# Performance work log

Measured on AMD Instinct MI355X. Metric: run time of the kernel, lower is better.

## Reference

```python
import jax, jax.numpy as jnp
import numpy as np

N = 100000       # num nodes
E = 1000000      # num edges
D_IN = 128       # input feature dim
D_H = 64         # hidden = output dim
EPS = 1e-5       # GraphNorm eps
SLOPE = 0.2      # LeakyReLU negative slope


def _glorot(key, shape):
    lim = float(np.sqrt(6.0 / (shape[0] + shape[1])))
    return jax.random.uniform(key, shape, jnp.float32, -lim, lim)


def setup_inputs() -> dict:
    key = jax.random.key(0)
    ks = jax.random.split(key, 6)
    return {
        "x": jax.random.normal(ks[0], (N, D_IN), jnp.float32),
        "edge_index": jax.random.randint(ks[1], (2, E), 0, N),
        "W_in": _glorot(ks[2], (D_IN, D_H)),
        "b_in": jnp.zeros((D_H,), jnp.float32),
        "W1": _glorot(ks[3], (D_H, D_H)),
        "b1": jnp.zeros((D_H,), jnp.float32),
        "gn1_alpha": jnp.ones((D_H,), jnp.float32),
        "gn1_gamma": jnp.ones((D_H,), jnp.float32),
        "gn1_beta": jnp.zeros((D_H,), jnp.float32),
        "W2": _glorot(ks[4], (D_H, D_H)),
        "b2": jnp.zeros((D_H,), jnp.float32),
        "gn2_alpha": jnp.ones((D_H,), jnp.float32),
        "gn2_gamma": jnp.ones((D_H,), jnp.float32),
        "gn2_beta": jnp.zeros((D_H,), jnp.float32),
    }


def gcn_conv(x, W, b, src, dst):
    # GCNConv with added self-loops and symmetric normalization:
    # out = D^{-1/2} (A + I) D^{-1/2} (x W) + b
    xw = x @ W                                                 # [N, D]
    ones = jnp.ones((src.shape[0],), x.dtype)
    deg = jax.ops.segment_sum(ones, dst, num_segments=x.shape[0]) + 1.0  # +1 self-loop
    dinv = jax.lax.rsqrt(deg)                                  # [N]
    coef = dinv[src] * dinv[dst]                               # [E]
    agg = jax.ops.segment_sum(xw[src] * coef[:, None], dst, num_segments=x.shape[0])
    return agg + xw * (dinv * dinv)[:, None] + b


def graph_norm(x, alpha, gamma, beta):
    # PyG GraphNorm over a single graph: per-feature mean/var over all nodes
    mean = jnp.mean(x, axis=0)
    c = x - alpha * mean
    var = jnp.mean(c * c, axis=0)
    return gamma * c * jax.lax.rsqrt(var + EPS) + beta


def reference(x, edge_index, W_in, b_in, W1, b1, gn1_alpha, gn1_gamma, gn1_beta,
              W2, b2, gn2_alpha, gn2_gamma, gn2_beta):
    src, dst = edge_index[0], edge_index[1]
    h = x @ W_in + b_in                                        # input projection
    h = graph_norm(gcn_conv(h, W1, b1, src, dst), gn1_alpha, gn1_gamma, gn1_beta)
    h = jnp.where(h > 0, h, SLOPE * h)                         # LeakyReLU(0.2); dropout=eval (identity)
    h = graph_norm(gcn_conv(h, W2, b2, src, dst), gn2_alpha, gn2_gamma, gn2_beta)
    return h                                                    # [N, D_H]
```

## Files before the change

### kernel.cpp

```cpp
#include <hip/hip_runtime.h>
#include <stdint.h>

#define N_NODES 100000
#define N_EDGES 1000000
#define D_IN 128
#define D_H 64
#define EPS 1e-5f
#define SLOPE 0.2f

typedef unsigned short u16;
typedef unsigned int u32;

__device__ __forceinline__ float bf2f(u16 u) {
    union { u32 i; float f; } v; v.i = ((u32)u) << 16; return v.f;
}
__device__ __forceinline__ u16 f2bf(float f) {
    union { float f; u32 i; } v; v.f = f;
    u32 r = (v.i + 0x7fffu + ((v.i >> 16) & 1u)) >> 16;
    return (u16)r;
}
__device__ __forceinline__ bool is_f32(const void* flagp) {
    return *(const u32*)flagp == 0x3F800000u;
}
__device__ __forceinline__ float loadf(const void* p, size_t i, bool m) {
    return m ? ((const float*)p)[i] : bf2f(((const u16*)p)[i]);
}

__global__ void kprep(const void* __restrict__ W_in, const void* __restrict__ b_in,
                      const void* __restrict__ W1, const void* __restrict__ flagp,
                      float* __restrict__ Wc, float* __restrict__ bc)
{
    bool m = is_f32(flagp);
    int c = blockIdx.x;
    int t = threadIdx.x;
    __shared__ float w1c[D_H];
    if (t < D_H) w1c[t] = loadf(W1, t * D_H + c, m);
    __syncthreads();
    float acc = 0.f;
    #pragma unroll 8
    for (int j = 0; j < D_H; j++) acc += loadf(W_in, t * D_H + j, m) * w1c[j];
    Wc[t * D_H + c] = acc;
    if (t == 0) {
        float b = 0.f;
        for (int j = 0; j < D_H; j++) b += loadf(b_in, j, m) * w1c[j];
        bc[c] = b;
    }
}

__global__ void kfill(const int* __restrict__ ei, int* __restrict__ cnt,
                      int* __restrict__ bucket)
{
    int e = blockIdx.x * blockDim.x + threadIdx.x;
    if (e >= N_EDGES) return;
    int s = ei[e];
    int d = ei[N_EDGES + e];
    int slot = atomicAdd(&cnt[d], 1);
    if (slot < 64) bucket[(size_t)d * 64 + slot] = s;
}

__global__ void kdinv(const int* __restrict__ cnt, float* __restrict__ dinv,
                      u16* __restrict__ xwb_pad)
{
    int i = blockIdx.x * blockDim.x + threadIdx.x;
    if (i < D_H) xwb_pad[(size_t)N_NODES * D_H + i] = 0;
    if (i >= N_NODES) return;
    dinv[i] = rsqrtf((float)cnt[i] + 1.0f);
}

__global__ __launch_bounds__(256) void kgemm1(const void* __restrict__ x,
        const float* __restrict__ Wc, const float* __restrict__ bc,
        const float* __restrict__ dinv, const void* __restrict__ flagp,
        u16* __restrict__ xwb)
{
    bool m = is_f32(flagp);
    __shared__ __align__(16) u16 xs[64 * 132];
    __shared__ float WL[D_IN * D_H];
    int tid = threadIdx.x;
    int row0 = blockIdx.x * 64;
    for (int i = tid; i < D_IN * D_H / 4; i += 256)
        ((float4*)WL)[i] = ((const float4*)Wc)[i];
    for (int i = tid; i < 64 * 32; i += 256) {
        int r = i >> 5, kq = (i & 31) * 4;
        int gr = row0 + r;
        ushort4 u = make_ushort4(0, 0, 0, 0);
        if (gr < N_NODES) {
            if (m) {
                float4 v = *(const float4*)((const float*)x + (size_t)gr * D_IN + kq);
                u = make_ushort4(f2bf(v.x), f2bf(v.y), f2bf(v.z), f2bf(v.w));
            } else {
                u = *(const ushort4*)((const u16*)x + (size_t)gr * D_IN + kq);
            }
        }
        *(ushort4*)(xs + r * 132 + kq) = u;
    }
    __syncthreads();
    int tx = tid & 15, ry = tid >> 4;
    float4 bcv = ((const float4*)bc)[tx];
    float acc[4][4];
    #pragma unroll
    for (int j = 0; j < 4; j++) { acc[j][0] = bcv.x; acc[j][1] = bcv.y; acc[j][2] = bcv.z; acc[j][3] = bcv.w; }
    #pragma unroll 4
    for (int k = 0; k < D_IN; k += 2) {
        float4 w0 = *(const float4*)(WL + k * D_H + tx * 4);
        float4 w1 = *(const float4*)(WL + (k + 1) * D_H + tx * 4);
        #pragma unroll
        for (int j = 0; j < 4; j++) {
            u32 p = *(const u32*)(xs + (ry * 4 + j) * 132 + k);
            float xl = bf2f((u16)(p & 0xffffu));
            float xh = bf2f((u16)(p >> 16));
            acc[j][0] += xl * w0.x; acc[j][1] += xl * w0.y; acc[j][2] += xl * w0.z; acc[j][3] += xl * w0.w;
            acc[j][0] += xh * w1.x; acc[j][1] += xh * w1.y; acc[j][2] += xh * w1.z; acc[j][3] += xh * w1.w;
        }
    }
    #pragma unroll
    for (int j = 0; j < 4; j++) {
        int gr = row0 + ry * 4 + j;
        if (gr < N_NODES) {
            float ds = dinv[gr];
            *(ushort4*)(xwb + (size_t)gr * D_H + tx * 4) =
                make_ushort4(f2bf(acc[j][0] * ds), f2bf(acc[j][1] * ds),
                             f2bf(acc[j][2] * ds), f2bf(acc[j][3] * ds));
        }
    }
}

__global__ __launch_bounds__(256) void kagg(const u16* __restrict__ xwb,
        const float* __restrict__ dinv, const int* __restrict__ cnt,
        const int* __restrict__ bucket, const void* __restrict__ bvec,
        const void* __restrict__ flagp, u16* __restrict__ ybuf,
        float* __restrict__ accum)
{
    bool m = is_f32(flagp);
    __shared__ int s_src[4][8][68];
    __shared__ __align__(16) float red[8][64];
    int tid = threadIdx.x;
    int wv = tid >> 6, L = tid & 63;
    int r = L >> 4, c = L & 15;
    int node0 = blockIdx.x * 32 + wv * 8;

    int cnt8 = cnt[node0 + (L & 7)];
    float di8 = dinv[node0 + (L & 7)];
    int deg[8]; float dd[8];
    #pragma unroll
    for (int t = 0; t < 8; t++) {
        deg[t] = min(__builtin_amdgcn_readlane(cnt8, t), 64);
        dd[t] = __uint_as_float(__builtin_amdgcn_readlane(__float_as_uint(di8), t));
    }
    #pragma unroll
    for (int t = 0; t < 8; t++) {
        int i = node0 + t;
        int sl = N_NODES;
        if (L < deg[t]) sl = bucket[(size_t)i * 64 + L];
        else if (L == deg[t]) sl = i;
        s_src[wv][t][L] = sl;
        if (L < 4) s_src[wv][t][64 + L] = (deg[t] == 64 && L == 0) ? i : N_NODES;
    }
    float b4[4];
    #pragma unroll
    for (int j = 0; j < 4; j++) b4[j] = loadf(bvec, c * 4 + j, m);

    float ls0 = 0, ls1 = 0, ls2 = 0, ls3 = 0;
    float lq0 = 0, lq1 = 0, lq2 = 0, lq3 = 0;

    #pragma unroll
    for (int tp = 0; tp < 8; tp += 2) {
        int na = deg[tp] + 1, nb = deg[tp + 1] + 1;
        int smax = max(na, nb);
        float a0 = 0, a1 = 0, a2 = 0, a3 = 0;
        float e0 = 0, e1 = 0, e2 = 0, e3 = 0;
        const int* sa = s_src[wv][tp];
        const int* sb = s_src[wv][tp + 1];
        for (int s = 0; s < smax; s += 4) {
            int ia = sa[s + r];
            int ib = sb[s + r];
            uint2 da = *(const uint2*)(xwb + (size_t)ia * D_H + c * 4);
            uint2 db = *(const uint2*)(xwb + (size_t)ib * D_H + c * 4);
            a0 += __uint_as_float(da.x << 16);
            a1 += __uint_as_float(da.x & 0xffff0000u);
            a2 += __uint_as_float(da.y << 16);
            a3 += __uint_as_float(da.y & 0xffff0000u);
            e0 += __uint_as_float(db.x << 16);
            e1 += __uint_as_float(db.x & 0xffff0000u);
            e2 += __uint_as_float(db.y << 16);
            e3 += __uint_as_float(db.y & 0xffff0000u);
        }
        a0 += __shfl_xor(a0, 16); a1 += __shfl_xor(a1, 16);
        a2 += __shfl_xor(a2, 16); a3 += __shfl_xor(a3, 16);
        e0 += __shfl_xor(e0, 16); e1 += __shfl_xor(e1, 16);
        e2 += __shfl_xor(e2, 16); e3 += __shfl_xor(e3, 16);
        a0 += __shfl_xor(a0, 32); a1 += __shfl_xor(a1, 32);
        a2 += __shfl_xor(a2, 32); a3 += __shfl_xor(a3, 32);
        e0 += __shfl_xor(e0, 32); e1 += __shfl_xor(e1, 32);
        e2 += __shfl_xor(e2, 32); e3 += __shfl_xor(e3, 32);
        float ya0 = dd[tp] * a0 + b4[0];
        float ya1 = dd[tp] * a1 + b4[1];
        float ya2 = dd[tp] * a2 + b4[2];
        float ya3 = dd[tp] * a3 + b4[3];
        float ye0 = dd[tp + 1] * e0 + b4[0];
        float ye1 = dd[tp + 1] * e1 + b4[1];
        float ye2 = dd[tp + 1] * e2 + b4[2];
        float ye3 = dd[tp + 1] * e3 + b4[3];
        if (r == 0) {
            *(ushort4*)(ybuf + (size_t)(node0 + tp) * D_H + c * 4) =
                make_ushort4(f2bf(ya0), f2bf(ya1), f2bf(ya2), f2bf(ya3));
            *(ushort4*)(ybuf + (size_t)(node0 + tp + 1) * D_H + c * 4) =
                make_ushort4(f2bf(ye0), f2bf(ye1), f2bf(ye2), f2bf(ye3));
            ls0 += ya0 + ye0; ls1 += ya1 + ye1;
            ls2 += ya2 + ye2; ls3 += ya3 + ye3;
            lq0 += ya0 * ya0 + ye0 * ye0; lq1 += ya1 * ya1 + ye1 * ye1;
            lq2 += ya2 * ya2 + ye2 * ye2; lq3 += ya3 * ya3 + ye3 * ye3;
        }
    }
    if (r == 0) {
        *(float4*)&red[wv * 2][c * 4] = make_float4(ls0, ls1, ls2, ls3);
        *(float4*)&red[wv * 2 + 1][c * 4] = make_float4(lq0, lq1, lq2, lq3);
    }
    __syncthreads();
    if (tid < 64) {
        atomicAdd(&accum[tid],      red[0][tid] + red[2][tid] + red[4][tid] + red[6][tid]);
        atomicAdd(&accum[64 + tid], red[1][tid] + red[3][tid] + red[5][tid] + red[7][tid]);
    }
}

__global__ void kparams(const float* __restrict__ accum, const void* __restrict__ alpha,
        const void* __restrict__ gamma, const void* __restrict__ beta,
        const void* __restrict__ flagp, float* __restrict__ params)
{
    bool m = is_f32(flagp);
    int f = threadIdx.x;
    float mean = accum[f] * (1.0f / N_NODES);
    float al = loadf(alpha, f, m);
    float var = accum[64 + f] * (1.0f / N_NODES) - mean * mean * al * (2.0f - al);
    var = fmaxf(var, 0.f);
    float a = loadf(gamma, f, m) * rsqrtf(var + EPS);
    params[f] = a;
    params[64 + f] = loadf(beta, f, m) - a * al * mean;
}

__global__ __launch_bounds__(256) void kgemm2(const u16* __restrict__ y1b,
        const void* __restrict__ W2, const float* __restrict__ params,
        const float* __restrict__ dinv, const void* __restrict__ flagp,
        u16* __restrict__ xwb)
{
    bool m = is_f32(flagp);
    __shared__ __align__(16) u16 hs[64 * 68];
    __shared__ float WL[D_H * D_H];
    __shared__ float aL[64], cL[64];
    int tid = threadIdx.x;
    if (tid < 64) { aL[tid] = params[tid]; cL[tid] = params[64 + tid]; }
    for (int i = tid; i < D_H * D_H; i += 256) WL[i] = loadf(W2, i, m);
    __syncthreads();
    int row0 = blockIdx.x * 64;
    for (int i = tid; i < 64 * 16; i += 256) {
        int r = i >> 4, kq = (i & 15) * 4;
        int gr = row0 + r;
        ushort4 u = make_ushort4(0, 0, 0, 0);
        if (gr < N_NODES) u = *(const ushort4*)(y1b + (size_t)gr * D_H + kq);
        float h0 = aL[kq + 0] * bf2f(u.x) + cL[kq + 0]; h0 = h0 > 0.f ? h0 : SLOPE * h0;
        float h1 = aL[kq + 1] * bf2f(u.y) + cL[kq + 1]; h1 = h1 > 0.f ? h1 : SLOPE * h1;
        float h2 = aL[kq + 2] * bf2f(u.z) + cL[kq + 2]; h2 = h2 > 0.f ? h2 : SLOPE * h2;
        float h3 = aL[kq + 3] * bf2f(u.w) + cL[kq + 3]; h3 = h3 > 0.f ? h3 : SLOPE * h3;
        *(ushort4*)(hs + r * 68 + kq) = make_ushort4(f2bf(h0), f2bf(h1), f2bf(h2), f2bf(h3));
    }
    __syncthreads();
    int tx = tid & 15, ry = tid >> 4;
    float acc[4][4] = {};
    #pragma unroll 4
    for (int k = 0; k < D_H; k += 2) {
        float4 w0 = *(const float4*)(WL + k * D_H + tx * 4);
        float4 w1 = *(const float4*)(WL + (k + 1) * D_H + tx * 4);
        #pragma unroll
        for (int j = 0; j < 4; j++) {
            u32 p = *(const u32*)(hs + (ry * 4 + j) * 68 + k);
            float xl = bf2f((u16)(p & 0xffffu));
            float xh = bf2f((u16)(p >> 16));
            acc[j][0] += xl * w0.x; acc[j][1] += xl * w0.y; acc[j][2] += xl * w0.z; acc[j][3] += xl * w0.w;
            acc[j][0] += xh * w1.x; acc[j][1] += xh * w1.y; acc[j][2] += xh * w1.z; acc[j][3] += xh * w1.w;
        }
    }
    #pragma unroll
    for (int j = 0; j < 4; j++) {
        int gr = row0 + ry * 4 + j;
        if (gr < N_NODES) {
            float ds = dinv[gr];
            *(ushort4*)(xwb + (size_t)gr * D_H + tx * 4) =
                make_ushort4(f2bf(acc[j][0] * ds), f2bf(acc[j][1] * ds),
                             f2bf(acc[j][2] * ds), f2bf(acc[j][3] * ds));
        }
    }
}

__global__ void kout(const u16* __restrict__ y2b, const float* __restrict__ params2,
                     const void* __restrict__ flagp, void* __restrict__ out)
{
    bool m = is_f32(flagp);
    int idx = blockIdx.x * blockDim.x + threadIdx.x;
    if (idx >= N_NODES * D_H) return;
    int f = idx & 63;
    float v = params2[f] * bf2f(y2b[idx]) + params2[64 + f];
    if (m) ((float*)out)[idx] = v;
    else   ((u16*)out)[idx] = f2bf(v);
}

extern "C" void kernel_launch(void* const* d_in, const int* in_sizes, int n_in,
                              void* d_out, int out_size, void* d_ws, size_t ws_size,
                              hipStream_t stream)
{
    const void* x    = d_in[0];
    const int*  ei   = (const int*)d_in[1];
    const void* W_in = d_in[2];
    const void* b_in = d_in[3];
    const void* W1   = d_in[4];
    const void* b1   = d_in[5];
    const void* gn1a = d_in[6];
    const void* gn1g = d_in[7];
    const void* gn1b = d_in[8];
    const void* W2   = d_in[9];
    const void* b2   = d_in[10];
    const void* gn2a = d_in[11];
    const void* gn2g = d_in[12];
    const void* gn2b = d_in[13];

    char* ws = (char*)d_ws;
    int*   cnt    = (int*)(ws + 0);
    float* accum  = (float*)(ws + 400000);
    float* params = (float*)(ws + 401024);
    float* bc     = (float*)(ws + 402048);
    float* Wc     = (float*)(ws + 402432);
    float* dinv   = (float*)(ws + 435200);
    int*   bucket = (int*)(ws + 1235200);
    u16*   bufA   = (u16*)(ws + 26835200);
    u16*   bufB   = (u16*)(ws + 39635456);

    hipMemsetAsync(ws, 0, 400000 + 1024, stream);

    kprep<<<64, 128, 0, stream>>>(W_in, b_in, W1, gn1a, Wc, bc);
    kfill<<<(N_EDGES + 255) / 256, 256, 0, stream>>>(ei, cnt, bucket);
    kdinv<<<(N_NODES + 255) / 256, 256, 0, stream>>>(cnt, dinv, bufA);
    kgemm1<<<(N_NODES + 63) / 64, 256, 0, stream>>>(x, Wc, bc, dinv, gn1a, bufA);
    kagg<<<N_NODES / 32, 256, 0, stream>>>(bufA, dinv, cnt, bucket, b1, gn1a, bufB, accum);
    kparams<<<1, 64, 0, stream>>>(accum, gn1a, gn1g, gn1b, gn1a, params);
    kgemm2<<<(N_NODES + 63) / 64, 256, 0, stream>>>(bufB, W2, params, dinv, gn1a, bufA);
    kagg<<<N_NODES / 32, 256, 0, stream>>>(bufA, dinv, cnt, bucket, b2, gn1a, bufB, accum + 128);
    kparams<<<1, 64, 0, stream>>>(accum + 128, gn2a, gn2g, gn2b, gn1a, params + 128);
    kout<<<(N_NODES * D_H + 255) / 256, 256, 0, stream>>>(bufB, params + 128, gn1a, d_out);
}
```

Before: 449.9 us.

## Prefetch first 16 neighbor rows per node into registers before aggregation

Measured after the change: 439.5 us. 2.3% less time.

```diff
diff --git a/kernel.cpp b/kernel.cpp
--- a/kernel.cpp
+++ b/kernel.cpp
@@ -131,7 +131,6 @@
         float* __restrict__ accum)
 {
     bool m = is_f32(flagp);
-    __shared__ int s_src[4][8][68];
     __shared__ __align__(16) float red[8][64];
     int tid = threadIdx.x;
     int wv = tid >> 6, L = tid & 63;
@@ -146,15 +145,31 @@
         deg[t] = min(__builtin_amdgcn_readlane(cnt8, t), 64);
         dd[t] = __uint_as_float(__builtin_amdgcn_readlane(__float_as_uint(di8), t));
     }
-    #pragma unroll
-    for (int t = 0; t < 8; t++) {
-        int i = node0 + t;
-        int sl = N_NODES;
-        if (L < deg[t]) sl = bucket[(size_t)i * 64 + L];
-        else if (L == deg[t]) sl = i;
-        s_src[wv][t][L] = sl;
-        if (L < 4) s_src[wv][t][64 + L] = (deg[t] == 64 && L == 0) ? i : N_NODES;
-    }
+
+    int bsl[8][4];
+    #pragma unroll
+    for (int t = 0; t < 8; t++) {
+        const int* bk = bucket + (size_t)(node0 + t) * 64;
+        #pragma unroll
+        for (int q = 0; q < 4; q++) bsl[t][q] = bk[q * 4 + r];
+    }
+    #pragma unroll
+    for (int t = 0; t < 8; t++) {
+        #pragma unroll
+        for (int q = 0; q < 4; q++) {
+            int si = q * 4 + r;
+            bsl[t][q] = (si < deg[t]) ? bsl[t][q]
+                      : ((si == deg[t]) ? (node0 + t) : N_NODES);
+        }
+    }
+    uint2 g[8][4];
+    #pragma unroll
+    for (int t = 0; t < 8; t++) {
+        #pragma unroll
+        for (int q = 0; q < 4; q++)
+            g[t][q] = *(const uint2*)(xwb + (size_t)bsl[t][q] * D_H + c * 4);
+    }
+
     float b4[4];
     #pragma unroll
     for (int j = 0; j < 4; j++) b4[j] = loadf(bvec, c * 4 + j, m);
@@ -163,52 +178,38 @@
     float lq0 = 0, lq1 = 0, lq2 = 0, lq3 = 0;
 
     #pragma unroll
-    for (int tp = 0; tp < 8; tp += 2) {
-        int na = deg[tp] + 1, nb = deg[tp + 1] + 1;
-        int smax = max(na, nb);
+    for (int t = 0; t < 8; t++) {
         float a0 = 0, a1 = 0, a2 = 0, a3 = 0;
-        float e0 = 0, e1 = 0, e2 = 0, e3 = 0;
-        const int* sa = s_src[wv][tp];
-        const int* sb = s_src[wv][tp + 1];
-        for (int s = 0; s < smax; s += 4) {
-            int ia = sa[s + r];
-            int ib = sb[s + r];
-            uint2 da = *(const uint2*)(xwb + (size_t)ia * D_H + c * 4);
-            uint2 db = *(const uint2*)(xwb + (size_t)ib * D_H + c * 4);
-            a0 += __uint_as_float(da.x << 16);
-            a1 += __uint_as_float(da.x & 0xffff0000u);
-            a2 += __uint_as_float(da.y << 16);
-            a3 += __uint_as_float(da.y & 0xffff0000u);
-            e0 += __uint_as_float(db.x << 16);
-            e1 += __uint_as_float(db.x & 0xffff0000u);
-            e2 += __uint_as_float(db.y << 16);
-            e3 += __uint_as_float(db.y & 0xffff0000u);
+        #pragma unroll
+        for (int q = 0; q < 4; q++) {
+            uint2 d = g[t][q];
+            a0 += __uint_as_float(d.x << 16);
+            a1 += __uint_as_float(d.x & 0xffff0000u);
+            a2 += __uint_as_float(d.y << 16);
+            a3 += __uint_as_float(d.y & 0xffff0000u);
+        }
+        int i = node0 + t;
+        for (int s = 16 + r; s <= deg[t]; s += 4) {
+            int sl = (s < deg[t]) ? bucket[(size_t)i * 64 + s] : i;
+            uint2 d = *(const uint2*)(xwb + (size_t)sl * D_H + c * 4);
+            a0 += __uint_as_float(d.x << 16);
+            a1 += __uint_as_float(d.x & 0xffff0000u);
+            a2 += __uint_as_float(d.y << 16);
+            a3 += __uint_as_float(d.y & 0xffff0000u);
         }
         a0 += __shfl_xor(a0, 16); a1 += __shfl_xor(a1, 16);
         a2 += __shfl_xor(a2, 16); a3 += __shfl_xor(a3, 16);
-        e0 += __shfl_xor(e0, 16); e1 += __shfl_xor(e1, 16);
-        e2 += __shfl_xor(e2, 16); e3 += __shfl_xor(e3, 16);
         a0 += __shfl_xor(a0, 32); a1 += __shfl_xor(a1, 32);
         a2 += __shfl_xor(a2, 32); a3 += __shfl_xor(a3, 32);
-        e0 += __shfl_xor(e0, 32); e1 += __shfl_xor(e1, 32);
-        e2 += __shfl_xor(e2, 32); e3 += __shfl_xor(e3, 32);
-        float ya0 = dd[tp] * a0 + b4[0];
-        float ya1 = dd[tp] * a1 + b4[1];
-        float ya2 = dd[tp] * a2 + b4[2];
-        float ya3 = dd[tp] * a3 + b4[3];
-        float ye0 = dd[tp + 1] * e0 + b4[0];
-        float ye1 = dd[tp + 1] * e1 + b4[1];
-        float ye2 = dd[tp + 1] * e2 + b4[2];
-        float ye3 = dd[tp + 1] * e3 + b4[3];
+        float y0 = dd[t] * a0 + b4[0];
+        float y1 = dd[t] * a1 + b4[1];
+        float y2 = dd[t] * a2 + b4[2];
+        float y3 = dd[t] * a3 + b4[3];
         if (r == 0) {
-            *(ushort4*)(ybuf + (size_t)(node0 + tp) * D_H + c * 4) =
-                make_ushort4(f2bf(ya0), f2bf(ya1), f2bf(ya2), f2bf(ya3));
-            *(ushort4*)(ybuf + (size_t)(node0 + tp + 1) * D_H + c * 4) =
-                make_ushort4(f2bf(ye0), f2bf(ye1), f2bf(ye2), f2bf(ye3));
-            ls0 += ya0 + ye0; ls1 += ya1 + ye1;
-            ls2 += ya2 + ye2; ls3 += ya3 + ye3;
-            lq0 += ya0 * ya0 + ye0 * ye0; lq1 += ya1 * ya1 + ye1 * ye1;
-            lq2 += ya2 * ya2 + ye2 * ye2; lq3 += ya3 * ya3 + ye3 * ye3;
+            *(ushort4*)(ybuf + (size_t)i * D_H + c * 4) =
+                make_ushort4(f2bf(y0), f2bf(y1), f2bf(y2), f2bf(y3));
+            ls0 += y0; ls1 += y1; ls2 += y2; ls3 += y3;
+            lq0 += y0 * y0; lq1 += y1 * y1; lq2 += y2 * y2; lq3 += y3 * y3;
         }
     }
     if (r == 0) {
```
